# Optimization experiments

Measured on AMD Instinct MI355X. Metric: run time of the kernel, lower is better.

## Reference

```python
import jax, jax.numpy as jnp
import numpy as np

D = 64      # size_in
RANK = 4    # rank
N = 262144  # batch of samples


def setup_inputs() -> dict:
    key = jax.random.key(0)
    k1, k2, k3, k4, k5 = jax.random.split(key, 5)
    s1 = 1.0 / np.sqrt(D)        # torch Linear init bound for linear1 (in=D)
    s2 = 1.0 / np.sqrt(2 * D)    # bound for linear2 (in=2D)
    return {
        "t": jnp.zeros((1,), dtype=jnp.float32),
        "input_": jax.random.normal(k1, (N, 2 * D), dtype=jnp.float32),
        "W1": jax.random.uniform(k2, (2 * D, D), jnp.float32, -s1, s1),
        "b1": jax.random.uniform(k3, (2 * D,), jnp.float32, -s1, s1),
        "W2": jax.random.uniform(k4, (RANK * D, 2 * D), jnp.float32, -s2, s2),
        "b2": jax.random.uniform(k5, (RANK * D,), jnp.float32, -s2, s2),
    }


def reference(t, input_, W1, b1, W2, b2):
    # Per-sample scalar Hamiltonian H(inp) = sum_j (v . W[:, j])^2 where
    # W = tanh(linear2(tanh(linear1(x)))).reshape(D, RANK); the torch einsum
    # 'mij,mhj,mi,mh->m' factors as sum_j (sum_i W[i,j] v[i])^2.
    def H(inp):
        x, v = inp[:D], inp[D:]
        h = jnp.tanh(W1 @ x + b1)                       # [2D]
        Wm = jnp.tanh(W2 @ h + b2).reshape(D, RANK)     # [D, RANK]
        return jnp.sum((v @ Wm) ** 2)

    # batch_jacobian of a scalar-per-sample fn == per-sample gradient [N, 2D]
    g = jax.vmap(jax.grad(H))(input_)
    dx = g[:, :D]
    dv = -g[:, D:]
    return jnp.concatenate([dx, dv], axis=-1)
```

## Files before the change

kernel.cpp:

```cpp
#include <hip/hip_runtime.h>

#define DD    64
#define TWOD  128
#define RD    256

typedef __attribute__((ext_vector_type(8))) short short8;
typedef __attribute__((ext_vector_type(4))) float float4v;
typedef __attribute__((ext_vector_type(4))) unsigned uint4v;
typedef unsigned long long ull;

__device__ __forceinline__ unsigned short f2b(float f) {
    unsigned u = __builtin_bit_cast(unsigned, f);
    u += 0x7fffu + ((u >> 16) & 1u);
    return (unsigned short)(u >> 16);
}
__device__ __forceinline__ float b2f(unsigned short s) {
    unsigned u = ((unsigned)s) << 16;
    return __builtin_bit_cast(float, u);
}
__device__ __forceinline__ unsigned cvt_pk_bf16(float lo, float hi) {
    unsigned r;
    asm("v_cvt_pk_bf16_f32 %0, %1, %2" : "=v"(r) : "v"(lo), "v"(hi));
    return r;
}
__device__ __forceinline__ float ftanh(float x) {
    float e = __expf(2.0f * x);
    return 1.0f - 2.0f / (e + 1.0f);
}
__device__ __forceinline__ void lds_fence() {
    asm volatile("s_waitcnt lgkmcnt(0)" ::: "memory");
}

__global__ void prep_weights(const float* __restrict__ W1, const float* __restrict__ W2,
                             unsigned short* __restrict__ wa, unsigned short* __restrict__ wd,
                             unsigned short* __restrict__ wb, unsigned short* __restrict__ wc) {
    int t = blockIdx.x * blockDim.x + threadIdx.x;
    if (t < 8192) {
        wa[t] = f2b(W1[t]);
        int c = t >> 7, r = t & 127;
        wd[t] = f2b(W1[r * 64 + c]);
    }
    if (t < 32768) {
        wb[t] = f2b(W2[t]);
        int c = t >> 8, k = t & 255;
        wc[t] = f2b(W2[k * 128 + c]);
    }
}

__global__ __launch_bounds__(64, 2) void geognn_kernel(
    const float* __restrict__ inp, const float* __restrict__ b1, const float* __restrict__ b2,
    const unsigned short* __restrict__ wa, const unsigned short* __restrict__ wd,
    const unsigned short* __restrict__ wb, const unsigned short* __restrict__ wc,
    float* __restrict__ out) {

    __shared__ __align__(16) unsigned short hd_s[2][16 * 264];
    __shared__ float v_s[2][16][68];
    __shared__ float4v y_s[2][16];

    const int  l   = threadIdx.x;
    const int  l15 = l & 15;
    const int  q   = l >> 4;
    const long row0 = (long)blockIdx.x * 32;

#pragma unroll
    for (int t = 0; t < 2; ++t)
#pragma unroll
        for (int r = 0; r < 16; ++r)
            v_s[t][r][l] = inp[(row0 + t * 16 + r) * TWOD + DD + l];

    short8 ax[2][2];
#pragma unroll
    for (int t = 0; t < 2; ++t)
#pragma unroll
        for (int kb = 0; kb < 2; ++kb) {
            const float4v* p = (const float4v*)(inp + (row0 + t * 16 + l15) * TWOD + kb * 32 + q * 8);
            float4v f0 = p[0], f1 = p[1];
            uint4v pk = { cvt_pk_bf16(f0.x, f0.y), cvt_pk_bf16(f0.z, f0.w),
                          cvt_pk_bf16(f1.x, f1.y), cvt_pk_bf16(f1.z, f1.w) };
            ax[t][kb] = __builtin_bit_cast(short8, pk);
        }

    float b1v[8];
#pragma unroll
    for (int nb = 0; nb < 8; ++nb) b1v[nb] = b1[nb * 16 + l15];
    float b2v[16];
#pragma unroll
    for (int nb = 0; nb < 16; ++nb) b2v[nb] = b2[nb * 16 + l15];

    short8 aw[16];
#pragma unroll
    for (int h = 0; h < 16; ++h)
        aw[h] = *(const short8*)(wa + ((h >> 1) * 16 + l15) * DD + (h & 1) * 32 + q * 8);

    unsigned g1p[2][16];
#pragma unroll
    for (int nb = 0; nb < 8; ++nb) {
        const int c = nb * 16 + l15;
#pragma unroll
        for (int t = 0; t < 2; ++t) {
            float4v acc = {0.f, 0.f, 0.f, 0.f};
            acc = __builtin_amdgcn_mfma_f32_16x16x32_bf16(ax[t][0], aw[nb * 2 + 0], acc, 0, 0, 0);
            acc = __builtin_amdgcn_mfma_f32_16x16x32_bf16(ax[t][1], aw[nb * 2 + 1], acc, 0, 0, 0);
#pragma unroll
            for (int i = 0; i < 4; i += 2) {
                float h0 = ftanh(acc[i]     + b1v[nb]);
                float h1 = ftanh(acc[i + 1] + b1v[nb]);
                hd_s[t][(q * 4 + i) * 136 + c]     = f2b(h0);
                hd_s[t][(q * 4 + i + 1) * 136 + c] = f2b(h1);
                g1p[t][nb * 2 + (i >> 1)] = cvt_pk_bf16(1.f - h0 * h0, 1.f - h1 * h1);
            }
        }
    }

    short8 bwA[8], bwB[8];
#pragma unroll
    for (int h = 0; h < 8; ++h)
        bwA[h] = *(const short8*)(wb + ((h >> 2) * 16 + l15) * TWOD + (h & 3) * 32 + q * 8);

    lds_fence();

    short8 ha[2][4];
#pragma unroll
    for (int t = 0; t < 2; ++t)
#pragma unroll
        for (int kb = 0; kb < 4; ++kb)
            ha[t][kb] = *(const short8*)(&hd_s[t][l15 * 136 + kb * 32 + q * 8]);

    lds_fence();

    float yp[2][4] = {{0.f, 0.f, 0.f, 0.f}, {0.f, 0.f, 0.f, 0.f}};
#pragma unroll
    for (int p = 0; p < 8; ++p) {
        short8* cur = (p & 1) ? bwB : bwA;
        short8* nxt = (p & 1) ? bwA : bwB;
        if (p < 7) {
#pragma unroll
            for (int h = 0; h < 8; ++h)
                nxt[h] = *(const short8*)(wb + (((p + 1) * 2 + (h >> 2)) * 16 + l15) * TWOD
                                          + (h & 3) * 32 + q * 8);
        }
#pragma unroll
        for (int s = 0; s < 2; ++s) {
            const int nb = p * 2 + s;
            const int n  = nb * 16 + l15;
#pragma unroll
            for (int t = 0; t < 2; ++t) {
                float4v acc = {0.f, 0.f, 0.f, 0.f};
#pragma unroll
                for (int kb = 0; kb < 4; ++kb)
                    acc = __builtin_amdgcn_mfma_f32_16x16x32_bf16(ha[t][kb], cur[s * 4 + kb], acc, 0, 0, 0);
#pragma unroll
                for (int i = 0; i < 4; ++i) {
                    const int r = q * 4 + i;
                    float u = ftanh(acc[i] + b2v[nb]);
                    hd_s[t][r * 264 + n] = f2b(u);
                    yp[t][i] += v_s[t][r][n >> 2] * u;
                }
            }
        }
    }

#pragma unroll
    for (int t = 0; t < 2; ++t)
#pragma unroll
        for (int i = 0; i < 4; ++i) {
            yp[t][i] += __shfl_xor(yp[t][i], 4, 64);
            yp[t][i] += __shfl_xor(yp[t][i], 8, 64);
        }
    if (l15 < 4) {
#pragma unroll
        for (int t = 0; t < 2; ++t)
#pragma unroll
            for (int i = 0; i < 4; ++i)
                ((float*)&y_s[t][q * 4 + i])[l15] = yp[t][i];
    }

    short8 cwA[8], cwB[8];
#pragma unroll
    for (int kb = 0; kb < 8; ++kb)
        cwA[kb] = *(const short8*)(wc + l15 * RD + kb * 32 + q * 8);

    lds_fence();

#pragma unroll
    for (int t = 0; t < 2; ++t)
#pragma unroll
        for (int r = 0; r < 16; ++r) {
            ull uu = *(const ull*)(&hd_s[t][r * 264 + 4 * l]);
            float4v y = y_s[t][r];
            float vv = v_s[t][r][l];
            float u0 = b2f((unsigned short)uu);
            float u1 = b2f((unsigned short)(uu >> 16));
            float u2 = b2f((unsigned short)(uu >> 32));
            float u3 = b2f((unsigned short)(uu >> 48));
            float dvv = y.x * u0 + y.y * u1 + y.z * u2 + y.w * u3;
            out[(row0 + t * 16 + r) * TWOD + DD + l] = -2.0f * dvv;
            float t0 = 2.0f * y.x * vv * (1.0f - u0 * u0);
            float t1 = 2.0f * y.y * vv * (1.0f - u1 * u1);
            float t2 = 2.0f * y.z * vv * (1.0f - u2 * u2);
            float t3 = 2.0f * y.w * vv * (1.0f - u3 * u3);
            unsigned w0 = cvt_pk_bf16(t0, t1);
            unsigned w1 = cvt_pk_bf16(t2, t3);
            ull w = (ull)w0 | ((ull)w1 << 32);
            *(ull*)(&hd_s[t][r * 264 + 4 * l]) = w;
        }

    lds_fence();

    short8 da[2][8];
#pragma unroll
    for (int t = 0; t < 2; ++t)
#pragma unroll
        for (int kb = 0; kb < 8; ++kb)
            da[t][kb] = *(const short8*)(&hd_s[t][l15 * 264 + kb * 32 + q * 8]);

    lds_fence();

#pragma unroll
    for (int nb = 0; nb < 8; ++nb) {
        short8* cur = (nb & 1) ? cwB : cwA;
        short8* nxt = (nb & 1) ? cwA : cwB;
        if (nb < 7) {
#pragma unroll
            for (int kb = 0; kb < 8; ++kb)
                nxt[kb] = *(const short8*)(wc + ((nb + 1) * 16 + l15) * RD + kb * 32 + q * 8);
        }
        const int c = nb * 16 + l15;
#pragma unroll
        for (int t = 0; t < 2; ++t) {
            float4v acc = {0.f, 0.f, 0.f, 0.f};
#pragma unroll
            for (int kb = 0; kb < 8; ++kb)
                acc = __builtin_amdgcn_mfma_f32_16x16x32_bf16(da[t][kb], cur[kb], acc, 0, 0, 0);
#pragma unroll
            for (int i = 0; i < 4; ++i) {
                unsigned short gh = (i & 1) ? (unsigned short)(g1p[t][nb * 2 + (i >> 1)] >> 16)
                                            : (unsigned short)(g1p[t][nb * 2 + (i >> 1)]);
                hd_s[t][(q * 4 + i) * 136 + c] = f2b(acc[i] * b2f(gh));
            }
        }
    }

    short8 dw[16];
#pragma unroll
    for (int h = 0; h < 16; ++h)
        dw[h] = *(const short8*)(wd + ((h >> 2) * 16 + l15) * TWOD + (h & 3) * 32 + q * 8);

    lds_fence();

    short8 dfa[2][4];
#pragma unroll
    for (int t = 0; t < 2; ++t)
#pragma unroll
        for (int kb = 0; kb < 4; ++kb)
            dfa[t][kb] = *(const short8*)(&hd_s[t][l15 * 136 + kb * 32 + q * 8]);
#pragma unroll
    for (int t = 0; t < 2; ++t)
#pragma unroll
        for (int nb = 0; nb < 4; ++nb) {
            float4v acc = {0.f, 0.f, 0.f, 0.f};
#pragma unroll
            for (int kb = 0; kb < 4; ++kb)
                acc = __builtin_amdgcn_mfma_f32_16x16x32_bf16(dfa[t][kb], dw[nb * 4 + kb], acc, 0, 0, 0);
#pragma unroll
            for (int i = 0; i < 4; ++i)
                out[(row0 + t * 16 + q * 4 + i) * TWOD + nb * 16 + l15] = acc[i];
        }
}

extern "C" void kernel_launch(void* const* d_in, const int* in_sizes, int n_in,
                              void* d_out, int out_size, void* d_ws, size_t ws_size,
                              hipStream_t stream) {
    const float* inp = (const float*)d_in[1];
    const float* W1  = (const float*)d_in[2];
    const float* b1  = (const float*)d_in[3];
    const float* W2  = (const float*)d_in[4];
    const float* b2  = (const float*)d_in[5];

    unsigned short* wa = (unsigned short*)d_ws;
    unsigned short* wd = wa + 8192;
    unsigned short* wb = wd + 8192;
    unsigned short* wc = wb + 32768;

    prep_weights<<<128, 256, 0, stream>>>(W1, W2, wa, wd, wb, wc);

    const int rows = in_sizes[1] / TWOD;
    geognn_kernel<<<rows / 32, 64, 0, stream>>>(inp, b1, b2, wa, wd, wb, wc,
                                                (float*)d_out);
}
```

Before: 361.2 us.

## Process three 16-row tiles per wave, store v in bf16, use raw exp/rcp tanh

Each single-wave block now handles three 16-row tiles instead of two, so every streamed weight fragment of W2 and its transpose feeds more MFMAs, and the last block is clamped to overlap the previous rows. The v vector is kept in LDS as bf16 to offset the extra tile's shared-memory cost, tanh now uses direct v_exp/v_rcp instructions, and pairs of bf16 values are packed with a single conversion. In exchange, register and LDS use per wave go up, which may lower occupancy, and v loses precision in the y accumulation and dx paths.

Result: faster. 345.8 us (-4.3%).

```diff
diff --git a/kernel.cpp b/kernel.cpp
--- a/kernel.cpp
+++ b/kernel.cpp
@@ -3,18 +3,20 @@
 #define DD    64
 #define TWOD  128
 #define RD    256
+#define NT    3
 
 typedef __attribute__((ext_vector_type(8))) short short8;
 typedef __attribute__((ext_vector_type(4))) float float4v;
 typedef __attribute__((ext_vector_type(4))) unsigned uint4v;
 typedef unsigned long long ull;
-
-__device__ __forceinline__ unsigned short f2b(float f) {
+typedef unsigned short ush;
+
+__device__ __forceinline__ ush f2b(float f) {
     unsigned u = __builtin_bit_cast(unsigned, f);
     u += 0x7fffu + ((u >> 16) & 1u);
-    return (unsigned short)(u >> 16);
-}
-__device__ __forceinline__ float b2f(unsigned short s) {
+    return (ush)(u >> 16);
+}
+__device__ __forceinline__ float b2f(ush s) {
     unsigned u = ((unsigned)s) << 16;
     return __builtin_bit_cast(float, u);
 }
@@ -23,17 +25,24 @@
     asm("v_cvt_pk_bf16_f32 %0, %1, %2" : "=v"(r) : "v"(lo), "v"(hi));
     return r;
 }
+__device__ __forceinline__ void store_pair(ush* p0, ush* p1, float lo, float hi) {
+    unsigned pk = cvt_pk_bf16(lo, hi);
+    *p0 = (ush)pk;
+    *p1 = (ush)(pk >> 16);
+}
 __device__ __forceinline__ float ftanh(float x) {
-    float e = __expf(2.0f * x);
-    return 1.0f - 2.0f / (e + 1.0f);
+    float e, r;
+    asm("v_exp_f32 %0, %1" : "=v"(e) : "v"(x * 2.885390082f));
+    asm("v_rcp_f32 %0, %1" : "=v"(r) : "v"(e + 1.0f));
+    return __builtin_fmaf(-2.0f, r, 1.0f);
 }
 __device__ __forceinline__ void lds_fence() {
     asm volatile("s_waitcnt lgkmcnt(0)" ::: "memory");
 }
 
 __global__ void prep_weights(const float* __restrict__ W1, const float* __restrict__ W2,
-                             unsigned short* __restrict__ wa, unsigned short* __restrict__ wd,
-                             unsigned short* __restrict__ wb, unsigned short* __restrict__ wc) {
+                             ush* __restrict__ wa, ush* __restrict__ wd,
+                             ush* __restrict__ wb, ush* __restrict__ wc) {
     int t = blockIdx.x * blockDim.x + threadIdx.x;
     if (t < 8192) {
         wa[t] = f2b(W1[t]);
@@ -49,28 +58,32 @@
 
 __global__ __launch_bounds__(64, 2) void geognn_kernel(
     const float* __restrict__ inp, const float* __restrict__ b1, const float* __restrict__ b2,
-    const unsigned short* __restrict__ wa, const unsigned short* __restrict__ wd,
-    const unsigned short* __restrict__ wb, const unsigned short* __restrict__ wc,
-    float* __restrict__ out) {
-
-    __shared__ __align__(16) unsigned short hd_s[2][16 * 264];
-    __shared__ float v_s[2][16][68];
-    __shared__ float4v y_s[2][16];
+    const ush* __restrict__ wa, const ush* __restrict__ wd,
+    const ush* __restrict__ wb, const ush* __restrict__ wc,
+    float* __restrict__ out, long nrows) {
+
+    __shared__ __align__(16) ush hd_s[NT][16 * 264];
+    __shared__ ush v_s[NT][16][68];
+    __shared__ float4v y_s[NT][16];
 
     const int  l   = threadIdx.x;
     const int  l15 = l & 15;
     const int  q   = l >> 4;
-    const long row0 = (long)blockIdx.x * 32;
-
-#pragma unroll
-    for (int t = 0; t < 2; ++t)
-#pragma unroll
-        for (int r = 0; r < 16; ++r)
-            v_s[t][r][l] = inp[(row0 + t * 16 + r) * TWOD + DD + l];
-
-    short8 ax[2][2];
-#pragma unroll
-    for (int t = 0; t < 2; ++t)
+    long row0 = (long)blockIdx.x * (16 * NT);
+    if (row0 + 16 * NT > nrows) row0 = nrows - 16 * NT;
+
+#pragma unroll
+    for (int t = 0; t < NT; ++t)
+#pragma unroll
+        for (int r = 0; r < 16; r += 2) {
+            float v0 = inp[(row0 + t * 16 + r)     * TWOD + DD + l];
+            float v1 = inp[(row0 + t * 16 + r + 1) * TWOD + DD + l];
+            store_pair(&v_s[t][r][l], &v_s[t][r + 1][l], v0, v1);
+        }
+
+    short8 ax[NT][2];
+#pragma unroll
+    for (int t = 0; t < NT; ++t)
 #pragma unroll
         for (int kb = 0; kb < 2; ++kb) {
             const float4v* p = (const float4v*)(inp + (row0 + t * 16 + l15) * TWOD + kb * 32 + q * 8);
@@ -92,12 +105,12 @@
     for (int h = 0; h < 16; ++h)
         aw[h] = *(const short8*)(wa + ((h >> 1) * 16 + l15) * DD + (h & 1) * 32 + q * 8);
 
-    unsigned g1p[2][16];
+    unsigned g1p[NT][16];
 #pragma unroll
     for (int nb = 0; nb < 8; ++nb) {
         const int c = nb * 16 + l15;
 #pragma unroll
-        for (int t = 0; t < 2; ++t) {
+        for (int t = 0; t < NT; ++t) {
             float4v acc = {0.f, 0.f, 0.f, 0.f};
             acc = __builtin_amdgcn_mfma_f32_16x16x32_bf16(ax[t][0], aw[nb * 2 + 0], acc, 0, 0, 0);
             acc = __builtin_amdgcn_mfma_f32_16x16x32_bf16(ax[t][1], aw[nb * 2 + 1], acc, 0, 0, 0);
@@ -105,8 +118,8 @@
             for (int i = 0; i < 4; i += 2) {
                 float h0 = ftanh(acc[i]     + b1v[nb]);
                 float h1 = ftanh(acc[i + 1] + b1v[nb]);
-                hd_s[t][(q * 4 + i) * 136 + c]     = f2b(h0);
-                hd_s[t][(q * 4 + i + 1) * 136 + c] = f2b(h1);
+                store_pair(&hd_s[t][(q * 4 + i) * 136 + c],
+                           &hd_s[t][(q * 4 + i + 1) * 136 + c], h0, h1);
                 g1p[t][nb * 2 + (i >> 1)] = cvt_pk_bf16(1.f - h0 * h0, 1.f - h1 * h1);
             }
         }
@@ -119,16 +132,16 @@
 
     lds_fence();
 
-    short8 ha[2][4];
-#pragma unroll
-    for (int t = 0; t < 2; ++t)
+    short8 ha[NT][4];
+#pragma unroll
+    for (int t = 0; t < NT; ++t)
 #pragma unroll
         for (int kb = 0; kb < 4; ++kb)
             ha[t][kb] = *(const short8*)(&hd_s[t][l15 * 136 + kb * 32 + q * 8]);
 
     lds_fence();
 
-    float yp[2][4] = {{0.f, 0.f, 0.f, 0.f}, {0.f, 0.f, 0.f, 0.f}};
+    float yp[NT][4] = {};
 #pragma unroll
     for (int p = 0; p < 8; ++p) {
         short8* cur = (p & 1) ? bwB : bwA;
@@ -143,25 +156,29 @@
         for (int s = 0; s < 2; ++s) {
             const int nb = p * 2 + s;
             const int n  = nb * 16 + l15;
-#pragma unroll
-            for (int t = 0; t < 2; ++t) {
+            const int c4 = nb * 4 + (l15 >> 2);
+#pragma unroll
+            for (int t = 0; t < NT; ++t) {
                 float4v acc = {0.f, 0.f, 0.f, 0.f};
 #pragma unroll
                 for (int kb = 0; kb < 4; ++kb)
                     acc = __builtin_amdgcn_mfma_f32_16x16x32_bf16(ha[t][kb], cur[s * 4 + kb], acc, 0, 0, 0);
-#pragma unroll
-                for (int i = 0; i < 4; ++i) {
-                    const int r = q * 4 + i;
-                    float u = ftanh(acc[i] + b2v[nb]);
-                    hd_s[t][r * 264 + n] = f2b(u);
-                    yp[t][i] += v_s[t][r][n >> 2] * u;
-                }
+                float u0 = ftanh(acc[0] + b2v[nb]);
+                float u1 = ftanh(acc[1] + b2v[nb]);
+                float u2 = ftanh(acc[2] + b2v[nb]);
+                float u3 = ftanh(acc[3] + b2v[nb]);
+                store_pair(&hd_s[t][(q * 4 + 0) * 264 + n], &hd_s[t][(q * 4 + 1) * 264 + n], u0, u1);
+                store_pair(&hd_s[t][(q * 4 + 2) * 264 + n], &hd_s[t][(q * 4 + 3) * 264 + n], u2, u3);
+                yp[t][0] += b2f(v_s[t][q * 4 + 0][c4]) * u0;
+                yp[t][1] += b2f(v_s[t][q * 4 + 1][c4]) * u1;
+                yp[t][2] += b2f(v_s[t][q * 4 + 2][c4]) * u2;
+                yp[t][3] += b2f(v_s[t][q * 4 + 3][c4]) * u3;
             }
         }
     }
 
 #pragma unroll
-    for (int t = 0; t < 2; ++t)
+    for (int t = 0; t < NT; ++t)
 #pragma unroll
         for (int i = 0; i < 4; ++i) {
             yp[t][i] += __shfl_xor(yp[t][i], 4, 64);
@@ -169,7 +186,7 @@
         }
     if (l15 < 4) {
 #pragma unroll
-        for (int t = 0; t < 2; ++t)
+        for (int t = 0; t < NT; ++t)
 #pragma unroll
             for (int i = 0; i < 4; ++i)
                 ((float*)&y_s[t][q * 4 + i])[l15] = yp[t][i];
@@ -183,16 +200,16 @@
     lds_fence();
 
 #pragma unroll
-    for (int t = 0; t < 2; ++t)
+    for (int t = 0; t < NT; ++t)
 #pragma unroll
         for (int r = 0; r < 16; ++r) {
             ull uu = *(const ull*)(&hd_s[t][r * 264 + 4 * l]);
             float4v y = y_s[t][r];
-            float vv = v_s[t][r][l];
-            float u0 = b2f((unsigned short)uu);
-            float u1 = b2f((unsigned short)(uu >> 16));
-            float u2 = b2f((unsigned short)(uu >> 32));
-            float u3 = b2f((unsigned short)(uu >> 48));
+            float vv = b2f(v_s[t][r][l]);
+            float u0 = b2f((ush)uu);
+            float u1 = b2f((ush)(uu >> 16));
+            float u2 = b2f((ush)(uu >> 32));
+            float u3 = b2f((ush)(uu >> 48));
             float dvv = y.x * u0 + y.y * u1 + y.z * u2 + y.w * u3;
             out[(row0 + t * 16 + r) * TWOD + DD + l] = -2.0f * dvv;
             float t0 = 2.0f * y.x * vv * (1.0f - u0 * u0);
@@ -207,9 +224,9 @@
 
     lds_fence();
 
-    short8 da[2][8];
-#pragma unroll
-    for (int t = 0; t < 2; ++t)
+    short8 da[NT][8];
+#pragma unroll
+    for (int t = 0; t < NT; ++t)
 #pragma unroll
         for (int kb = 0; kb < 8; ++kb)
             da[t][kb] = *(const short8*)(&hd_s[t][l15 * 264 + kb * 32 + q * 8]);
@@ -227,17 +244,18 @@
         }
         const int c = nb * 16 + l15;
 #pragma unroll
-        for (int t = 0; t < 2; ++t) {
+        for (int t = 0; t < NT; ++t) {
             float4v acc = {0.f, 0.f, 0.f, 0.f};
 #pragma unroll
             for (int kb = 0; kb < 8; ++kb)
                 acc = __builtin_amdgcn_mfma_f32_16x16x32_bf16(da[t][kb], cur[kb], acc, 0, 0, 0);
-#pragma unroll
-            for (int i = 0; i < 4; ++i) {
-                unsigned short gh = (i & 1) ? (unsigned short)(g1p[t][nb * 2 + (i >> 1)] >> 16)
-                                            : (unsigned short)(g1p[t][nb * 2 + (i >> 1)]);
-                hd_s[t][(q * 4 + i) * 136 + c] = f2b(acc[i] * b2f(gh));
-            }
+            unsigned glo = g1p[t][nb * 2 + 0], ghi = g1p[t][nb * 2 + 1];
+            float d0 = acc[0] * b2f((ush)glo);
+            float d1 = acc[1] * b2f((ush)(glo >> 16));
+            float d2 = acc[2] * b2f((ush)ghi);
+            float d3 = acc[3] * b2f((ush)(ghi >> 16));
+            store_pair(&hd_s[t][(q * 4 + 0) * 136 + c], &hd_s[t][(q * 4 + 1) * 136 + c], d0, d1);
+            store_pair(&hd_s[t][(q * 4 + 2) * 136 + c], &hd_s[t][(q * 4 + 3) * 136 + c], d2, d3);
         }
     }
 
@@ -248,14 +266,14 @@
 
     lds_fence();
 
-    short8 dfa[2][4];
-#pragma unroll
-    for (int t = 0; t < 2; ++t)
+    short8 dfa[NT][4];
+#pragma unroll
+    for (int t = 0; t < NT; ++t)
 #pragma unroll
         for (int kb = 0; kb < 4; ++kb)
             dfa[t][kb] = *(const short8*)(&hd_s[t][l15 * 136 + kb * 32 + q * 8]);
 #pragma unroll
-    for (int t = 0; t < 2; ++t)
+    for (int t = 0; t < NT; ++t)
 #pragma unroll
         for (int nb = 0; nb < 4; ++nb) {
             float4v acc = {0.f, 0.f, 0.f, 0.f};
@@ -277,14 +295,15 @@
     const float* W2  = (const float*)d_in[4];
     const float* b2  = (const float*)d_in[5];
 
-    unsigned short* wa = (unsigned short*)d_ws;
-    unsigned short* wd = wa + 8192;
-    unsigned short* wb = wd + 8192;
-    unsigned short* wc = wb + 32768;
+    ush* wa = (ush*)d_ws;
+    ush* wd = wa + 8192;
+    ush* wb = wd + 8192;
+    ush* wc = wb + 32768;
 
     prep_weights<<<128, 256, 0, stream>>>(W1, W2, wa, wd, wb, wc);
 
-    const int rows = in_sizes[1] / TWOD;
-    geognn_kernel<<<rows / 32, 64, 0, stream>>>(inp, b1, b2, wa, wd, wb, wc,
-                                                (float*)d_out);
-}
+    const long rows = in_sizes[1] / TWOD;
+    const int  grid = (int)((rows + 16 * NT - 1) / (16 * NT));
+    geognn_kernel<<<grid, 64, 0, stream>>>(inp, b1, b2, wa, wd, wb, wc,
+                                           (float*)d_out, rows);
+}
```
